# Optimization experiments

Measured on AMD Instinct MI355X. Metric: run time of the kernel, lower is better.

Reference implementation:

```python
import jax, jax.numpy as jnp
import numpy as np

DIM = 384
HEADS = 12
HEAD_DIM = DIM // HEADS
SCALE = HEAD_DIM ** -0.5
HIDDEN = 4 * DIM
EPS = 1e-5


def _dwconv(x, w, b):
    # depthwise 3x3 conv, NCHW, kernel [C,1,3,3], groups=C
    y = jax.lax.conv_general_dilated(
        x, w, window_strides=(1, 1), padding='SAME',
        dimension_numbers=('NCHW', 'OIHW', 'NCHW'),
        feature_group_count=x.shape[1])
    return y + b[None, :, None, None]


def _layernorm(x, g, b):
    mu = jnp.mean(x, axis=-1, keepdims=True)
    var = jnp.mean(jnp.square(x - mu), axis=-1, keepdims=True)
    return (x - mu) * jax.lax.rsqrt(var + EPS) * g + b


def setup_inputs() -> dict:
    key = jax.random.key(0)
    ks = jax.random.split(key, 10)
    s = 0.02
    inp = {
        'x': jax.random.normal(ks[0], (32, DIM, 28, 28), dtype=jnp.float32),
        'cpe1_w': jax.random.normal(ks[1], (DIM, 1, 3, 3), dtype=jnp.float32) * s,
        'cpe1_b': jnp.zeros((DIM,), jnp.float32),
        'norm1_g': jnp.ones((DIM,), jnp.float32),
        'norm1_b': jnp.zeros((DIM,), jnp.float32),
        'qkv_w': jax.random.normal(ks[2], (3 * DIM, DIM), dtype=jnp.float32) * s,
        'proj_w': jax.random.normal(ks[3], (DIM, DIM), dtype=jnp.float32) * s,
        'proj_b': jnp.zeros((DIM,), jnp.float32),
        'cpe2_w': jax.random.normal(ks[4], (DIM, 1, 3, 3), dtype=jnp.float32) * s,
        'cpe2_b': jnp.zeros((DIM,), jnp.float32),
        'norm2_g': jnp.ones((DIM,), jnp.float32),
        'norm2_b': jnp.zeros((DIM,), jnp.float32),
        'fc1_w': jax.random.normal(ks[5], (HIDDEN, DIM), dtype=jnp.float32) * s,
        'fc1_b': jnp.zeros((HIDDEN,), jnp.float32),
        'fc2_w': jax.random.normal(ks[6], (DIM, HIDDEN), dtype=jnp.float32) * s,
        'fc2_b': jnp.zeros((DIM,), jnp.float32),
    }
    return inp


def reference(x, cpe1_w, cpe1_b, norm1_g, norm1_b, qkv_w, proj_w, proj_b,
              cpe2_w, cpe2_b, norm2_g, norm2_b, fc1_w, fc1_b, fc2_w, fc2_b):
    B, C, H, W = x.shape
    N = H * W
    # cpe1: depthwise conv residual (act = Identity)
    x = x + _dwconv(x, cpe1_w, cpe1_b)
    x = jnp.transpose(x.reshape(B, C, N), (0, 2, 1))  # [B, N, C]

    # channel attention
    cur = _layernorm(x, norm1_g, norm1_b)
    qkv = cur @ qkv_w.T  # [B, N, 3C]
    qkv = qkv.reshape(B, N, 3, HEADS, HEAD_DIM)
    q = qkv[:, :, 0]  # [B, N, h, d]
    k = qkv[:, :, 1] * SCALE
    v = qkv[:, :, 2]
    # attn = k^T @ v over tokens: [B, h, d, d]
    attn = jnp.einsum('bnhd,bnhe->bhde', k, v)
    attn = jax.nn.softmax(attn, axis=-1)
    # out[n,d] = sum_e attn[d,e] * q[n,e]
    out = jnp.einsum('bhde,bnhe->bnhd', attn, q).reshape(B, N, C)
    cur = out @ proj_w.T + proj_b
    x = x + cur

    # cpe2
    x = jnp.transpose(x, (0, 2, 1)).reshape(B, C, H, W)
    x = x + _dwconv(x, cpe2_w, cpe2_b)

    # MLP
    x = jnp.transpose(x.reshape(B, C, N), (0, 2, 1))  # [B, N, C]
    y = _layernorm(x, norm2_g, norm2_b)
    y = jax.nn.gelu(y @ fc1_w.T + fc1_b, approximate=False)
    y = y @ fc2_w.T + fc2_b
    x = x + y
    return jnp.transpose(x, (0, 2, 1)).reshape(B, C, H, W)
```

## Files before the change

### kernel.cpp

```cpp
#include <hip/hip_runtime.h>
#include <hip/hip_bf16.h>

#define CDIM 384
#define NHEADS 12
#define HDIM 32
#define HIDDEN 1536
#define BBATCH 32
#define HH 28
#define WW 28
#define NTOK 784
#define BN (BBATCH * NTOK)
#define LN_EPS 1e-5f
#define ATT_SCALE 0.17677669529663687f
#define YTILES 196
#define PERXCD 25

typedef __hip_bfloat16 bf16;
typedef __attribute__((ext_vector_type(8))) short bf16x8;
typedef __attribute__((ext_vector_type(4))) float f32x4;

__device__ __forceinline__ void stf(float* p, float v) { *p = v; }
__device__ __forceinline__ void stf(bf16* p, float v) { *p = __float2bfloat16(v); }

__device__ __forceinline__ short f2bs(float v) {
    bf16 t = __float2bfloat16(v);
    return *reinterpret_cast<short*>(&t);
}

__device__ __forceinline__ float gelu_f(float x) {
    float u = x * (0.7978845608f + 0.0356774081f * x * x);
    float e = __expf(-2.f * u);
    return x / (1.f + e);
}

__device__ __forceinline__ void gload16(const void* g, void* l) {
    __builtin_amdgcn_global_load_lds(
        (const __attribute__((address_space(1))) unsigned int*)g,
        (__attribute__((address_space(3))) unsigned int*)l, 16, 0, 0);
}

__global__ __launch_bounds__(256) void prep_k(
    const float* __restrict__ w0, const float* __restrict__ w1,
    const float* __restrict__ w2, const float* __restrict__ w3,
    bf16* __restrict__ dst, const float* __restrict__ cw,
    float* __restrict__ cwt)
{
    int blk = blockIdx.x;
    if (blk >= 6912) {
        int i = (blk - 6912) * 256 + threadIdx.x;
        if (i < 9 * CDIM) {
            int k = i / CDIM, c = i % CDIM;
            cwt[i] = cw[c * 9 + k];
        }
        return;
    }
    int i = blk * 256 + threadIdx.x;
    const float* src; int off;
    if (i < 442368)       { src = w0; off = i; }
    else if (i < 589824)  { src = w1; off = i - 442368; }
    else if (i < 1179648) { src = w2; off = i - 589824; }
    else                  { src = w3; off = i - 1179648; }
    dst[i] = __float2bfloat16(src[off]);
}

__global__ __launch_bounds__(256) void dwconv_nchw_plane(
    const float* __restrict__ x, const float* __restrict__ w,
    const float* __restrict__ bias, float* __restrict__ y)
{
    __shared__ float sm[NTOK];
    int bc = blockIdx.x;
    int c = bc % CDIM;
    const float* xp = x + (size_t)bc * NTOK;
    int tid = threadIdx.x;
#pragma unroll
    for (int i = 0; i < 4; i++) {
        int p = tid + i * 256;
        if (p < NTOK) sm[p] = xp[p];
    }
    __syncthreads();
    const float* wp = w + c * 9;
    float w00 = wp[0], w01 = wp[1], w02 = wp[2];
    float w10 = wp[3], w11 = wp[4], w12 = wp[5];
    float w20 = wp[6], w21 = wp[7], w22 = wp[8];
    float bc_ = bias[c];
    float* yp = y + (size_t)bc * NTOK;
#pragma unroll
    for (int i = 0; i < 4; i++) {
        int p = tid + i * 256;
        if (p >= NTOK) break;
        int h = p / WW, wcol = p % WW;
        bool hm = h > 0, hp = h < HH - 1, wm = wcol > 0, wpv = wcol < WW - 1;
        float s = w11 * sm[p];
        if (hm)        s += w01 * sm[p - WW];
        if (hp)        s += w21 * sm[p + WW];
        if (wm)        s += w10 * sm[p - 1];
        if (wpv)       s += w12 * sm[p + 1];
        if (hm && wm)  s += w00 * sm[p - WW - 1];
        if (hm && wpv) s += w02 * sm[p - WW + 1];
        if (hp && wm)  s += w20 * sm[p + WW - 1];
        if (hp && wpv) s += w22 * sm[p + WW + 1];
        yp[p] = sm[p] + s + bc_;
    }
}

__global__ __launch_bounds__(256) void transpose_in(
    const float* __restrict__ in, float* __restrict__ out)
{
    __shared__ float t[32][33];
    int b = blockIdx.z;
    int n0 = blockIdx.y * 32;
    int c0 = blockIdx.x * 32;
    int tx = threadIdx.x, ty = threadIdx.y;
    for (int i = ty; i < 32; i += 8) {
        int n = n0 + tx;
        if (n < NTOK) t[i][tx] = in[((size_t)b * CDIM + c0 + i) * NTOK + n];
    }
    __syncthreads();
    for (int i = ty; i < 32; i += 8) {
        int n = n0 + i;
        if (n < NTOK) out[((size_t)b * NTOK + n) * CDIM + c0 + tx] = t[tx][i];
    }
}

template <typename TO>
__global__ __launch_bounds__(256) void layernorm_k(
    const float* __restrict__ in, const float* __restrict__ g,
    const float* __restrict__ b, TO* __restrict__ out)
{
    int wid = threadIdx.x >> 6;
    int lane = threadIdx.x & 63;
    size_t r = (size_t)blockIdx.x * 4 + wid;
    const float* row = in + r * CDIM;
    float v[6];
    float s = 0.f;
#pragma unroll
    for (int j = 0; j < 6; j++) { v[j] = row[lane + 64 * j]; s += v[j]; }
#pragma unroll
    for (int off = 32; off >= 1; off >>= 1) s += __shfl_xor(s, off);
    float mu = s * (1.f / CDIM);
    float q = 0.f;
#pragma unroll
    for (int j = 0; j < 6; j++) { float d = v[j] - mu; q += d * d; }
#pragma unroll
    for (int off = 32; off >= 1; off >>= 1) q += __shfl_xor(q, off);
    float rs = rsqrtf(q * (1.f / CDIM) + LN_EPS);
    TO* orow = out + r * CDIM;
#pragma unroll
    for (int j = 0; j < 6; j++) {
        int c = lane + 64 * j;
        stf(&orow[c], (v[j] - mu) * rs * g[c] + b[c]);
    }
}

__global__ __launch_bounds__(256) void cpe2_ln_fused(
    const float* __restrict__ xin, const float* __restrict__ wt,
    const float* __restrict__ cbias, const float* __restrict__ g,
    const float* __restrict__ b, float* __restrict__ x3,
    bf16* __restrict__ lnout)
{
    __shared__ float wts[9 * CDIM];
    int tid = threadIdx.x;
    for (int i = tid; i < 9 * CDIM; i += 256) wts[i] = wt[i];
    __syncthreads();
    int wid = tid >> 6, lane = tid & 63;
    int tok = blockIdx.x * 4 + wid;
    int n = tok % NTOK;
    int h = n / WW, w = n % WW;
    bool hm = h > 0, hp = h < HH - 1, wm = w > 0, wpv = w < WW - 1;
    const float* row = xin + (size_t)tok * CDIM;
    float ctr[6], acc6[6], val[6];
#pragma unroll
    for (int j = 0; j < 6; j++) {
        int c = lane + 64 * j;
        ctr[j] = row[c];
        acc6[j] = wts[4 * CDIM + c] * ctr[j];
    }
#define TAP(k, cond, dn)                                                      \
    if (cond) {                                                               \
        const float* rp = row + (dn) * CDIM;                                  \
        _Pragma("unroll")                                                     \
        for (int j = 0; j < 6; j++) {                                         \
            int c = lane + 64 * j;                                            \
            acc6[j] = fmaf(wts[(k) * CDIM + c], rp[c], acc6[j]);              \
        }                                                                     \
    }
    TAP(0, hm && wm,   -WW - 1)
    TAP(1, hm,         -WW)
    TAP(2, hm && wpv,  -WW + 1)
    TAP(3, wm,         -1)
    TAP(5, wpv,        1)
    TAP(6, hp && wm,   WW - 1)
    TAP(7, hp,         WW)
    TAP(8, hp && wpv,  WW + 1)
#undef TAP
    float s = 0.f;
    float* x3row = x3 + (size_t)tok * CDIM;
#pragma unroll
    for (int j = 0; j < 6; j++) {
        int c = lane + 64 * j;
        val[j] = ctr[j] + acc6[j] + cbias[c];
        x3row[c] = val[j];
        s += val[j];
    }
#pragma unroll
    for (int off = 32; off >= 1; off >>= 1) s += __shfl_xor(s, off);
    float mu = s * (1.f / CDIM);
    float q = 0.f;
#pragma unroll
    for (int j = 0; j < 6; j++) { float d = val[j] - mu; q += d * d; }
#pragma unroll
    for (int off = 32; off >= 1; off >>= 1) q += __shfl_xor(q, off);
    float rs = rsqrtf(q * (1.f / CDIM) + LN_EPS);
    bf16* orow = lnout + (size_t)tok * CDIM;
#pragma unroll
    for (int j = 0; j < 6; j++) {
        int c = lane + 64 * j;
        orow[c] = __float2bfloat16((val[j] - mu) * rs * g[c] + b[c]);
    }
}

template <int ACT, bool RES, typename TO, bool OUTT, int K>
__global__ __launch_bounds__(256, 4) void gemm_mfma(
    const short* __restrict__ Abf, const short* __restrict__ Bw,
    const float* __restrict__ bias, const float* __restrict__ res,
    TO* __restrict__ Co, int M, int NX)
{
    int id = blockIdx.x;
    int xcd = id & 7, slot_ = id >> 3;
    int yloc = slot_ / NX, xx = slot_ - yloc * NX;
    int y = xcd * PERXCD + yloc;
    if (y >= YTILES) return;

    __shared__ __align__(16) short lds[16896];
    const int tid = threadIdx.x;
    const int wid = tid >> 6, lane = tid & 63;
    const int wrow = wid >> 1, wcol = wid & 1;
    const int quad = lane >> 4, lr = lane & 15;
    const int r0 = y * 128, m0 = xx * 128;

    const int srow = lane >> 2;
    const int sg   = (lane & 3) ^ ((lane >> 3) & 3);
    const short* gA = Abf + (size_t)(r0 + wid * 32 + srow) * K + sg * 8;
    const short* gB = Bw  + (size_t)(m0 + wid * 32 + srow) * K + sg * 8;

    auto stage = [&](int k0, int p) {
        short* lA = lds + p * 8192 + wid * 1024;
        short* lB = lds + p * 8192 + 4096 + wid * 1024;
#pragma unroll
        for (int k = 0; k < 2; k++) {
            gload16(gA + k0 + (size_t)k * 16 * K, lA + k * 512);
            gload16(gB + k0 + (size_t)k * 16 * K, lB + k * 512);
        }
    };

    const int slot = (quad ^ ((lr >> 1) & 3)) * 8;
    int fA[4], fB[4];
#pragma unroll
    for (int i = 0; i < 4; i++) {
        fA[i] = (wrow * 64 + i * 16 + lr) * 32 + slot;
        fB[i] = 4096 + (wcol * 64 + i * 16 + lr) * 32 + slot;
    }

    f32x4 acc[4][4] = {};

    stage(0, 0);
    int p = 0;
    for (int k0 = 0; k0 < K; k0 += 32) {
        __syncthreads();
        if (k0 + 32 < K) stage(k0 + 32, p ^ 1);
        const short* As = lds + p * 8192;
        bf16x8 av[4], bv[4];
#pragma unroll
        for (int i = 0; i < 4; i++) {
            av[i] = *(const bf16x8*)(As + fA[i]);
            bv[i] = *(const bf16x8*)(As + fB[i]);
        }
#pragma unroll
        for (int i = 0; i < 4; i++)
#pragma unroll
            for (int j = 0; j < 4; j++)
                acc[i][j] = __builtin_amdgcn_mfma_f32_16x16x32_bf16(
                    av[i], bv[j], acc[i][j], 0, 0, 0);
        p ^= 1;
    }

    if constexpr (OUTT) {
        float* Csf = (float*)lds;
        __syncthreads();
#pragma unroll
        for (int pass = 0; pass < 2; pass++) {
            if (wcol == pass) {
#pragma unroll
                for (int i = 0; i < 4; i++) {
                    int lrow = wrow * 64 + i * 16 + quad * 4;
#pragma unroll
                    for (int j = 0; j < 4; j++) {
                        int lcol = j * 16 + lr;
                        int gc = m0 + pass * 64 + lcol;
                        float bb = bias ? bias[gc] : 0.f;
#pragma unroll
                        for (int rr = 0; rr < 4; rr++) {
                            float v = acc[i][j][rr] + bb;
                            if (RES)
                                v += res[(size_t)(r0 + lrow + rr) * M + gc];
                            if (ACT == 1) v = gelu_f(v);
                            Csf[(lrow + rr) * 66 + lcol] = v;
                        }
                    }
                }
            }
            __syncthreads();
            int tok = tid & 127;
            int csel = tid >> 7;
            int gtok = r0 + tok;
            int bb2 = gtok / NTOK;
            int nn2 = gtok - bb2 * NTOK;
#pragma unroll
            for (int s = 0; s < 32; s++) {
                int cl = s * 2 + csel;
                int gcol = m0 + pass * 64 + cl;
                Co[((size_t)bb2 * CDIM + gcol) * NTOK + nn2] = Csf[tok * 66 + cl];
            }
            __syncthreads();
        }
    } else if constexpr (sizeof(TO) == 4) {
#pragma unroll
        for (int i = 0; i < 4; i++) {
            int gr = r0 + wrow * 64 + i * 16 + quad * 4;
#pragma unroll
            for (int j = 0; j < 4; j++) {
                int gc = m0 + wcol * 64 + j * 16 + lr;
                float bb = bias ? bias[gc] : 0.f;
#pragma unroll
                for (int rr = 0; rr < 4; rr++) {
                    size_t idx = (size_t)(gr + rr) * M + gc;
                    float v = acc[i][j][rr] + bb;
                    if (RES) v += res[idx];
                    if (ACT == 1) v = gelu_f(v);
                    stf((float*)&Co[idx], v);
                }
            }
        }
    } else {
        __syncthreads();
        short* Cs = lds;
#pragma unroll
        for (int i = 0; i < 4; i++) {
            int lrow = wrow * 64 + i * 16 + quad * 4;
#pragma unroll
            for (int j = 0; j < 4; j++) {
                int lcol = wcol * 64 + j * 16 + lr;
                float bb = bias ? bias[m0 + lcol] : 0.f;
#pragma unroll
                for (int rr = 0; rr < 4; rr++) {
                    float v = acc[i][j][rr] + bb;
                    if (ACT == 1) v = gelu_f(v);
                    Cs[(lrow + rr) * 132 + lcol] = f2bs(v);
                }
            }
        }
        __syncthreads();
        short* co = (short*)Co;
#pragma unroll
        for (int s = 0; s < 16; s++) {
            int row = s * 8 + (tid >> 5);
            int seg = tid & 31;
            uint2 vv = *(const uint2*)(Cs + row * 132 + seg * 4);
            *(uint2*)(co + (size_t)(r0 + row) * M + m0 + seg * 4) = vv;
        }
    }
}

__global__ __launch_bounds__(256) void attn_k(
    const bf16* __restrict__ qkv, float* __restrict__ attn)
{
    int bh = blockIdx.x;
    int b = bh / NHEADS, h = bh % NHEADS;
    __shared__ float ks[64][32];
    __shared__ float vs[64][32];
    __shared__ float sm[32][33];
    int tid = threadIdx.x;
    int d = tid >> 3, e0 = (tid & 7) * 4;
    float acc[4] = {0.f, 0.f, 0.f, 0.f};
    for (int n0 = 0; n0 < NTOK; n0 += 64) {
#pragma unroll
        for (int i = 0; i < 8; i++) {
            int idx = tid + i * 256;
            int nn = idx >> 5, cc = idx & 31;
            int n = n0 + nn;
            float kv = 0.f, vv = 0.f;
            if (n < NTOK) {
                size_t base = ((size_t)b * NTOK + n) * (3 * CDIM);
                kv = ATT_SCALE * __bfloat162float(qkv[base + CDIM + h * HDIM + cc]);
                vv = __bfloat162float(qkv[base + 2 * CDIM + h * HDIM + cc]);
            }
            ks[nn][cc] = kv; vs[nn][cc] = vv;
        }
        __syncthreads();
#pragma unroll 8
        for (int nn = 0; nn < 64; nn++) {
            float kd = ks[nn][d];
            float4 vv4 = *(const float4*)&vs[nn][e0];
            acc[0] = fmaf(kd, vv4.x, acc[0]);
            acc[1] = fmaf(kd, vv4.y, acc[1]);
            acc[2] = fmaf(kd, vv4.z, acc[2]);
            acc[3] = fmaf(kd, vv4.w, acc[3]);
        }
        __syncthreads();
    }
#pragma unroll
    for (int j = 0; j < 4; j++) sm[d][e0 + j] = acc[j];
    __syncthreads();
    if (tid < 32) {
        float mx = -1e30f;
#pragma unroll
        for (int e = 0; e < 32; e++) mx = fmaxf(mx, sm[tid][e]);
        float ssum = 0.f;
        float ex[32];
#pragma unroll
        for (int e = 0; e < 32; e++) { ex[e] = expf(sm[tid][e] - mx); ssum += ex[e]; }
        float inv = 1.f / ssum;
        float* arow = attn + ((size_t)bh * 32 + tid) * 32;
#pragma unroll
        for (int e = 0; e < 32; e++) arow[e] = ex[e] * inv;
    }
}

__global__ __launch_bounds__(384) void apply_attn_k(
    const bf16* __restrict__ qkv, const float* __restrict__ attn,
    bf16* __restrict__ out)
{
    int b = blockIdx.x;
    int chunk = blockIdx.y;
    int tid = threadIdx.x;
    int h = tid >> 5;
    __shared__ float qs[8][CDIM];
    float at[32];
    const float4* ap = (const float4*)(attn + ((size_t)(b * NHEADS) * 32 + tid) * 32);
#pragma unroll
    for (int e4 = 0; e4 < 8; e4++) {
        float4 v = ap[e4];
        at[e4 * 4 + 0] = v.x; at[e4 * 4 + 1] = v.y;
        at[e4 * 4 + 2] = v.z; at[e4 * 4 + 3] = v.w;
    }
    int nbase = chunk * 56;
    for (int t0 = 0; t0 < 56; t0 += 8) {
        __syncthreads();
#pragma unroll
        for (int i = 0; i < 8; i++) {
            int n = nbase + t0 + i;
            qs[i][tid] = __bfloat162float(qkv[((size_t)b * NTOK + n) * (3 * CDIM) + tid]);
        }
        __syncthreads();
#pragma unroll
        for (int i = 0; i < 8; i++) {
            const float4* q4 = (const float4*)&qs[i][h * 32];
            float s = 0.f;
#pragma unroll
            for (int e4 = 0; e4 < 8; e4++) {
                float4 qv = q4[e4];
                s = fmaf(at[e4 * 4 + 0], qv.x, s);
                s = fmaf(at[e4 * 4 + 1], qv.y, s);
                s = fmaf(at[e4 * 4 + 2], qv.z, s);
                s = fmaf(at[e4 * 4 + 3], qv.w, s);
            }
            int n = nbase + t0 + i;
            out[((size_t)b * NTOK + n) * CDIM + tid] = __float2bfloat16(s);
        }
    }
}

extern "C" void kernel_launch(void* const* d_in, const int* in_sizes, int n_in,
                              void* d_out, int out_size, void* d_ws, size_t ws_size,
                              hipStream_t stream) {
    const float* x      = (const float*)d_in[0];
    const float* cpe1_w = (const float*)d_in[1];
    const float* cpe1_b = (const float*)d_in[2];
    const float* n1g    = (const float*)d_in[3];
    const float* n1b    = (const float*)d_in[4];
    const float* qkv_w  = (const float*)d_in[5];
    const float* proj_w = (const float*)d_in[6];
    const float* proj_b = (const float*)d_in[7];
    const float* cpe2_w = (const float*)d_in[8];
    const float* cpe2_b = (const float*)d_in[9];
    const float* n2g    = (const float*)d_in[10];
    const float* n2b    = (const float*)d_in[11];
    const float* fc1_w  = (const float*)d_in[12];
    const float* fc1_b  = (const float*)d_in[13];
    const float* fc2_w  = (const float*)d_in[14];
    const float* fc2_b  = (const float*)d_in[15];

    const size_t A = (size_t)BN * CDIM;
    const size_t HA = A / 2;

    bf16* wqkv  = (bf16*)d_ws;
    bf16* wproj = wqkv + 442368;
    bf16* wfc1  = wproj + 147456;
    bf16* wfc2  = wfc1 + 589824;
    float* base = (float*)d_ws + 884736;

    float* xt        = base;
    bf16*  curb      = (bf16*)(base + A);
    bf16*  ylnb      = (bf16*)(base + A);
    bf16*  qkvb      = (bf16*)(base + A + HA);
    float* x3        = base + A + HA;
    bf16*  h1        = (bf16*)(base + A + HA + A);
    float* attnm     = base + 3 * A;
    bf16*  attn_outb = (bf16*)(base + 3 * A + 393216);
    float* xconv     = base + (A * 7) / 2;
    float* cpe2_wt   = base + (A * 9) / 2;

    const int GEMM_GRID3  = 8 * PERXCD * 3;
    const int GEMM_GRID9  = 8 * PERXCD * 9;
    const int GEMM_GRID12 = 8 * PERXCD * 12;

    prep_k<<<6926, 256, 0, stream>>>(qkv_w, proj_w, fc1_w, fc2_w, wqkv,
                                     cpe2_w, cpe2_wt);

    dwconv_nchw_plane<<<BBATCH * CDIM, 256, 0, stream>>>(x, cpe1_w, cpe1_b, xconv);
    transpose_in<<<dim3(CDIM / 32, (NTOK + 31) / 32, BBATCH), dim3(32, 8), 0, stream>>>(
        xconv, xt);
    layernorm_k<bf16><<<BN / 4, 256, 0, stream>>>(xt, n1g, n1b, curb);
    gemm_mfma<0, false, bf16, false, 384><<<GEMM_GRID9, 256, 0, stream>>>(
        (const short*)curb, (const short*)wqkv, nullptr, nullptr, qkvb, 1152, 9);
    attn_k<<<BBATCH * NHEADS, 256, 0, stream>>>(qkvb, attnm);
    apply_attn_k<<<dim3(BBATCH, 14), 384, 0, stream>>>(qkvb, attnm, attn_outb);
    gemm_mfma<0, true, float, false, 384><<<GEMM_GRID3, 256, 0, stream>>>(
        (const short*)attn_outb, (const short*)wproj, proj_b, xt, xt, 384, 3);
    cpe2_ln_fused<<<BN / 4, 256, 0, stream>>>(xt, cpe2_wt, cpe2_b, n2g, n2b,
                                              x3, ylnb);
    gemm_mfma<1, false, bf16, false, 384><<<GEMM_GRID12, 256, 0, stream>>>(
        (const short*)ylnb, (const short*)wfc1, fc1_b, nullptr, h1, 1536, 12);
    gemm_mfma<0, true, float, true, 1536><<<GEMM_GRID3, 256, 0, stream>>>(
        (const short*)h1, (const short*)wfc2, fc2_b, x3, (float*)d_out, 384, 3);
}
```

Measured before the change: 438.5 us.

## Fuse cpe1 conv with transpose and vectorize LN, cpe2, attention loads

Merges the first depthwise conv into the NCHW-to-NHWC transpose kernel by loading a 96-token halo window per channel into shared memory, which removes the intermediate xconv buffer round trip and one launch. LayerNorm1 and the cpe2+LN kernel switch to half-wave rows with float4 loads and packed bf16 stores. The attention reduction and attention-apply kernels now load bf16 K/V/Q in 16-byte vectors and convert with shifts. The cost is extra halo reads and branchy conv work in the transpose kernel.

```diff
diff --git a/kernel.cpp b/kernel.cpp
--- a/kernel.cpp
+++ b/kernel.cpp
@@ -27,6 +27,10 @@
     return *reinterpret_cast<short*>(&t);
 }
 
+__device__ __forceinline__ float bf2f(unsigned short u) {
+    return __uint_as_float(((unsigned)u) << 16);
+}
+
 __device__ __forceinline__ float gelu_f(float x) {
     float u = x * (0.7978845608f + 0.0356774081f * x * x);
     float e = __expf(-2.f * u);
@@ -63,92 +67,95 @@
     dst[i] = __float2bfloat16(src[off]);
 }
 
-__global__ __launch_bounds__(256) void dwconv_nchw_plane(
+__global__ __launch_bounds__(256) void cpe1_tr_fused(
     const float* __restrict__ x, const float* __restrict__ w,
-    const float* __restrict__ bias, float* __restrict__ y)
-{
-    __shared__ float sm[NTOK];
-    int bc = blockIdx.x;
-    int c = bc % CDIM;
-    const float* xp = x + (size_t)bc * NTOK;
-    int tid = threadIdx.x;
-#pragma unroll
-    for (int i = 0; i < 4; i++) {
-        int p = tid + i * 256;
-        if (p < NTOK) sm[p] = xp[p];
-    }
-    __syncthreads();
-    const float* wp = w + c * 9;
-    float w00 = wp[0], w01 = wp[1], w02 = wp[2];
-    float w10 = wp[3], w11 = wp[4], w12 = wp[5];
-    float w20 = wp[6], w21 = wp[7], w22 = wp[8];
-    float bc_ = bias[c];
-    float* yp = y + (size_t)bc * NTOK;
-#pragma unroll
-    for (int i = 0; i < 4; i++) {
-        int p = tid + i * 256;
-        if (p >= NTOK) break;
-        int h = p / WW, wcol = p % WW;
-        bool hm = h > 0, hp = h < HH - 1, wm = wcol > 0, wpv = wcol < WW - 1;
-        float s = w11 * sm[p];
-        if (hm)        s += w01 * sm[p - WW];
-        if (hp)        s += w21 * sm[p + WW];
-        if (wm)        s += w10 * sm[p - 1];
-        if (wpv)       s += w12 * sm[p + 1];
-        if (hm && wm)  s += w00 * sm[p - WW - 1];
-        if (hm && wpv) s += w02 * sm[p - WW + 1];
-        if (hp && wm)  s += w20 * sm[p + WW - 1];
-        if (hp && wpv) s += w22 * sm[p + WW + 1];
-        yp[p] = sm[p] + s + bc_;
-    }
-}
-
-__global__ __launch_bounds__(256) void transpose_in(
-    const float* __restrict__ in, float* __restrict__ out)
-{
+    const float* __restrict__ bias, float* __restrict__ xt)
+{
+    __shared__ float sm[32][100];
     __shared__ float t[32][33];
     int b = blockIdx.z;
     int n0 = blockIdx.y * 32;
     int c0 = blockIdx.x * 32;
     int tx = threadIdx.x, ty = threadIdx.y;
-    for (int i = ty; i < 32; i += 8) {
-        int n = n0 + tx;
-        if (n < NTOK) t[i][tx] = in[((size_t)b * CDIM + c0 + i) * NTOK + n];
+    int wstart = n0 - 32;
+    for (int ci = ty; ci < 32; ci += 8) {
+        const float* bp = x + ((size_t)b * CDIM + c0 + ci) * NTOK;
+#pragma unroll
+        for (int j = 0; j < 3; j++) {
+            int l = tx + j * 32;
+            int n = wstart + l;
+            sm[ci][l] = ((unsigned)n < NTOK) ? bp[n] : 0.f;
+        }
+    }
+    __syncthreads();
+    int n = n0 + tx;
+    if (n < NTOK) {
+        int h = n / WW, wc = n % WW;
+        bool hm = h > 0, hp = h < HH - 1, wm = wc > 0, wpv = wc < WW - 1;
+        int l = tx + 32;
+        for (int ci = ty; ci < 32; ci += 8) {
+            const float* wp = w + (c0 + ci) * 9;
+            float s = wp[4] * sm[ci][l];
+            if (hm)        s += wp[1] * sm[ci][l - WW];
+            if (hp)        s += wp[7] * sm[ci][l + WW];
+            if (wm)        s += wp[3] * sm[ci][l - 1];
+            if (wpv)       s += wp[5] * sm[ci][l + 1];
+            if (hm && wm)  s += wp[0] * sm[ci][l - WW - 1];
+            if (hm && wpv) s += wp[2] * sm[ci][l - WW + 1];
+            if (hp && wm)  s += wp[6] * sm[ci][l + WW - 1];
+            if (hp && wpv) s += wp[8] * sm[ci][l + WW + 1];
+            t[tx][ci] = sm[ci][l] + s + bias[c0 + ci];
+        }
     }
     __syncthreads();
     for (int i = ty; i < 32; i += 8) {
-        int n = n0 + i;
-        if (n < NTOK) out[((size_t)b * NTOK + n) * CDIM + c0 + tx] = t[tx][i];
-    }
-}
-
-template <typename TO>
-__global__ __launch_bounds__(256) void layernorm_k(
+        int nn = n0 + i;
+        if (nn < NTOK)
+            xt[((size_t)b * NTOK + nn) * CDIM + c0 + tx] = t[i][tx];
+    }
+}
+
+__global__ __launch_bounds__(256) void ln1_k(
     const float* __restrict__ in, const float* __restrict__ g,
-    const float* __restrict__ b, TO* __restrict__ out)
-{
-    int wid = threadIdx.x >> 6;
-    int lane = threadIdx.x & 63;
-    size_t r = (size_t)blockIdx.x * 4 + wid;
-    const float* row = in + r * CDIM;
-    float v[6];
+    const float* __restrict__ b, bf16* __restrict__ out)
+{
+    int tid = threadIdx.x;
+    int l = tid & 31;
+    size_t tok = (size_t)blockIdx.x * 8 + (tid >> 5);
+    const float4* row = (const float4*)(in + tok * CDIM);
+    float4 v[3];
     float s = 0.f;
 #pragma unroll
-    for (int j = 0; j < 6; j++) { v[j] = row[lane + 64 * j]; s += v[j]; }
-#pragma unroll
-    for (int off = 32; off >= 1; off >>= 1) s += __shfl_xor(s, off);
+    for (int j = 0; j < 3; j++) {
+        v[j] = row[l + j * 32];
+        s += v[j].x + v[j].y + v[j].z + v[j].w;
+    }
+#pragma unroll
+    for (int off = 16; off >= 1; off >>= 1) s += __shfl_xor(s, off);
     float mu = s * (1.f / CDIM);
     float q = 0.f;
 #pragma unroll
-    for (int j = 0; j < 6; j++) { float d = v[j] - mu; q += d * d; }
-#pragma unroll
-    for (int off = 32; off >= 1; off >>= 1) q += __shfl_xor(q, off);
+    for (int j = 0; j < 3; j++) {
+        float dx = v[j].x - mu, dy = v[j].y - mu;
+        float dz = v[j].z - mu, dw = v[j].w - mu;
+        q += dx * dx + dy * dy + dz * dz + dw * dw;
+    }
+#pragma unroll
+    for (int off = 16; off >= 1; off >>= 1) q += __shfl_xor(q, off);
     float rs = rsqrtf(q * (1.f / CDIM) + LN_EPS);
-    TO* orow = out + r * CDIM;
-#pragma unroll
-    for (int j = 0; j < 6; j++) {
-        int c = lane + 64 * j;
-        stf(&orow[c], (v[j] - mu) * rs * g[c] + b[c]);
+    const float4* g4 = (const float4*)g;
+    const float4* b4 = (const float4*)b;
+    ushort4* o4 = (ushort4*)(out + tok * CDIM);
+#pragma unroll
+    for (int j = 0; j < 3; j++) {
+        int idx = l + j * 32;
+        float4 gv = g4[idx], bv = b4[idx];
+        ushort4 r;
+        r.x = (unsigned short)f2bs((v[j].x - mu) * rs * gv.x + bv.x);
+        r.y = (unsigned short)f2bs((v[j].y - mu) * rs * gv.y + bv.y);
+        r.z = (unsigned short)f2bs((v[j].z - mu) * rs * gv.z + bv.z);
+        r.w = (unsigned short)f2bs((v[j].w - mu) * rs * gv.w + bv.w);
+        o4[idx] = r;
     }
 }
 
@@ -160,29 +167,38 @@
 {
     __shared__ float wts[9 * CDIM];
     int tid = threadIdx.x;
-    for (int i = tid; i < 9 * CDIM; i += 256) wts[i] = wt[i];
+    for (int i = tid; i < 864; i += 256)
+        ((float4*)wts)[i] = ((const float4*)wt)[i];
     __syncthreads();
-    int wid = tid >> 6, lane = tid & 63;
-    int tok = blockIdx.x * 4 + wid;
-    int n = tok % NTOK;
-    int h = n / WW, w = n % WW;
-    bool hm = h > 0, hp = h < HH - 1, wm = w > 0, wpv = w < WW - 1;
-    const float* row = xin + (size_t)tok * CDIM;
-    float ctr[6], acc6[6], val[6];
-#pragma unroll
-    for (int j = 0; j < 6; j++) {
-        int c = lane + 64 * j;
-        ctr[j] = row[c];
-        acc6[j] = wts[4 * CDIM + c] * ctr[j];
-    }
-#define TAP(k, cond, dn)                                                      \
-    if (cond) {                                                               \
-        const float* rp = row + (dn) * CDIM;                                  \
-        _Pragma("unroll")                                                     \
-        for (int j = 0; j < 6; j++) {                                         \
-            int c = lane + 64 * j;                                            \
-            acc6[j] = fmaf(wts[(k) * CDIM + c], rp[c], acc6[j]);              \
-        }                                                                     \
+    int l = tid & 31;
+    size_t tok = (size_t)blockIdx.x * 8 + (tid >> 5);
+    int n = (int)(tok % NTOK);
+    int h = n / WW, wc = n % WW;
+    bool hm = h > 0, hp = h < HH - 1, wm = wc > 0, wpv = wc < WW - 1;
+    const float* row = xin + tok * CDIM;
+    const float4* w4 = (const float4*)wts;
+    float4 ctr[3], acc[3];
+#pragma unroll
+    for (int j = 0; j < 3; j++) {
+        int idx = l + j * 32;
+        ctr[j] = ((const float4*)row)[idx];
+        float4 ww = w4[4 * 96 + idx];
+        acc[j].x = ww.x * ctr[j].x; acc[j].y = ww.y * ctr[j].y;
+        acc[j].z = ww.z * ctr[j].z; acc[j].w = ww.w * ctr[j].w;
+    }
+#define TAP(k, cond, dn)                                                     \
+    if (cond) {                                                              \
+        const float4* rp = (const float4*)(row + (dn) * CDIM);               \
+        _Pragma("unroll")                                                    \
+        for (int j = 0; j < 3; j++) {                                        \
+            int idx = l + j * 32;                                            \
+            float4 vv = rp[idx];                                             \
+            float4 ww = w4[(k) * 96 + idx];                                  \
+            acc[j].x = fmaf(ww.x, vv.x, acc[j].x);                           \
+            acc[j].y = fmaf(ww.y, vv.y, acc[j].y);                           \
+            acc[j].z = fmaf(ww.z, vv.z, acc[j].z);                           \
+            acc[j].w = fmaf(ww.w, vv.w, acc[j].w);                           \
+        }                                                                    \
     }
     TAP(0, hm && wm,   -WW - 1)
     TAP(1, hm,         -WW)
@@ -194,28 +210,45 @@
     TAP(8, hp && wpv,  WW + 1)
 #undef TAP
     float s = 0.f;
-    float* x3row = x3 + (size_t)tok * CDIM;
-#pragma unroll
-    for (int j = 0; j < 6; j++) {
-        int c = lane + 64 * j;
-        val[j] = ctr[j] + acc6[j] + cbias[c];
-        x3row[c] = val[j];
-        s += val[j];
-    }
-#pragma unroll
-    for (int off = 32; off >= 1; off >>= 1) s += __shfl_xor(s, off);
+    float4 val[3];
+    float4* x3r = (float4*)(x3 + tok * CDIM);
+#pragma unroll
+    for (int j = 0; j < 3; j++) {
+        int idx = l + j * 32;
+        float4 cb = ((const float4*)cbias)[idx];
+        val[j].x = ctr[j].x + acc[j].x + cb.x;
+        val[j].y = ctr[j].y + acc[j].y + cb.y;
+        val[j].z = ctr[j].z + acc[j].z + cb.z;
+        val[j].w = ctr[j].w + acc[j].w + cb.w;
+        x3r[idx] = val[j];
+        s += val[j].x + val[j].y + val[j].z + val[j].w;
+    }
+#pragma unroll
+    for (int off = 16; off >= 1; off >>= 1) s += __shfl_xor(s, off);
     float mu = s * (1.f / CDIM);
     float q = 0.f;
 #pragma unroll
-    for (int j = 0; j < 6; j++) { float d = val[j] - mu; q += d * d; }
-#pragma unroll
-    for (int off = 32; off >= 1; off >>= 1) q += __shfl_xor(q, off);
+    for (int j = 0; j < 3; j++) {
+        float dx = val[j].x - mu, dy = val[j].y - mu;
+        float dz = val[j].z - mu, dw = val[j].w - mu;
+        q += dx * dx + dy * dy + dz * dz + dw * dw;
+    }
+#pragma unroll
+    for (int off = 16; off >= 1; off >>= 1) q += __shfl_xor(q, off);
     float rs = rsqrtf(q * (1.f / CDIM) + LN_EPS);
-    bf16* orow = lnout + (size_t)tok * CDIM;
-#pragma unroll
-    for (int j = 0; j < 6; j++) {
-        int c = lane + 64 * j;
-        orow[c] = __float2bfloat16((val[j] - mu) * rs * g[c] + b[c]);
+    const float4* g4 = (const float4*)g;
+    const float4* b4 = (const float4*)b;
+    ushort4* o4 = (ushort4*)(lnout + tok * CDIM);
+#pragma unroll
+    for (int j = 0; j < 3; j++) {
+        int idx = l + j * 32;
+        float4 gv = g4[idx], bv = b4[idx];
+        ushort4 r;
+        r.x = (unsigned short)f2bs((val[j].x - mu) * rs * gv.x + bv.x);
+        r.y = (unsigned short)f2bs((val[j].y - mu) * rs * gv.y + bv.y);
+        r.z = (unsigned short)f2bs((val[j].z - mu) * rs * gv.z + bv.z);
+        r.w = (unsigned short)f2bs((val[j].w - mu) * rs * gv.w + bv.w);
+        o4[idx] = r;
     }
 }
 
@@ -381,26 +414,36 @@
     __shared__ float sm[32][33];
     int tid = threadIdx.x;
     int d = tid >> 3, e0 = (tid & 7) * 4;
+    int nn = tid >> 2, q8 = (tid & 3) * 8;
     float acc[4] = {0.f, 0.f, 0.f, 0.f};
     for (int n0 = 0; n0 < NTOK; n0 += 64) {
-#pragma unroll
-        for (int i = 0; i < 8; i++) {
-            int idx = tid + i * 256;
-            int nn = idx >> 5, cc = idx & 31;
-            int n = n0 + nn;
-            float kv = 0.f, vv = 0.f;
-            if (n < NTOK) {
-                size_t base = ((size_t)b * NTOK + n) * (3 * CDIM);
-                kv = ATT_SCALE * __bfloat162float(qkv[base + CDIM + h * HDIM + cc]);
-                vv = __bfloat162float(qkv[base + 2 * CDIM + h * HDIM + cc]);
+        int n = n0 + nn;
+        float kv[8], vv[8];
+        if (n < NTOK) {
+            const unsigned short* base =
+                (const unsigned short*)qkv + ((size_t)b * NTOK + n) * (3 * CDIM);
+            uint4 kq = *(const uint4*)(base + CDIM + h * HDIM + q8);
+            uint4 vq = *(const uint4*)(base + 2 * CDIM + h * HDIM + q8);
+            const unsigned short* kp = (const unsigned short*)&kq;
+            const unsigned short* vp = (const unsigned short*)&vq;
+#pragma unroll
+            for (int j = 0; j < 8; j++) {
+                kv[j] = ATT_SCALE * bf2f(kp[j]);
+                vv[j] = bf2f(vp[j]);
             }
-            ks[nn][cc] = kv; vs[nn][cc] = vv;
-        }
+        } else {
+#pragma unroll
+            for (int j = 0; j < 8; j++) { kv[j] = 0.f; vv[j] = 0.f; }
+        }
+        *(float4*)&ks[nn][q8]     = make_float4(kv[0], kv[1], kv[2], kv[3]);
+        *(float4*)&ks[nn][q8 + 4] = make_float4(kv[4], kv[5], kv[6], kv[7]);
+        *(float4*)&vs[nn][q8]     = make_float4(vv[0], vv[1], vv[2], vv[3]);
+        *(float4*)&vs[nn][q8 + 4] = make_float4(vv[4], vv[5], vv[6], vv[7]);
         __syncthreads();
 #pragma unroll 8
-        for (int nn = 0; nn < 64; nn++) {
-            float kd = ks[nn][d];
-            float4 vv4 = *(const float4*)&vs[nn][e0];
+        for (int k = 0; k < 64; k++) {
+            float kd = ks[k][d];
+            float4 vv4 = *(const float4*)&vs[k][e0];
             acc[0] = fmaf(kd, vv4.x, acc[0]);
             acc[1] = fmaf(kd, vv4.y, acc[1]);
             acc[2] = fmaf(kd, vv4.z, acc[2]);
@@ -443,13 +486,21 @@
         at[e4 * 4 + 0] = v.x; at[e4 * 4 + 1] = v.y;
         at[e4 * 4 + 2] = v.z; at[e4 * 4 + 3] = v.w;
     }
+    int row8 = tid / 48;
+    int seg = tid - row8 * 48;
     int nbase = chunk * 56;
     for (int t0 = 0; t0 < 56; t0 += 8) {
         __syncthreads();
-#pragma unroll
-        for (int i = 0; i < 8; i++) {
-            int n = nbase + t0 + i;
-            qs[i][tid] = __bfloat162float(qkv[((size_t)b * NTOK + n) * (3 * CDIM) + tid]);
+        {
+            int n = nbase + t0 + row8;
+            const unsigned short* src =
+                (const unsigned short*)qkv + ((size_t)b * NTOK + n) * (3 * CDIM) + seg * 8;
+            uint4 qv = *(const uint4*)src;
+            const unsigned short* qp = (const unsigned short*)&qv;
+            *(float4*)&qs[row8][seg * 8] =
+                make_float4(bf2f(qp[0]), bf2f(qp[1]), bf2f(qp[2]), bf2f(qp[3]));
+            *(float4*)&qs[row8][seg * 8 + 4] =
+                make_float4(bf2f(qp[4]), bf2f(qp[5]), bf2f(qp[6]), bf2f(qp[7]));
         }
         __syncthreads();
 #pragma unroll
@@ -507,7 +558,6 @@
     bf16*  h1        = (bf16*)(base + A + HA + A);
     float* attnm     = base + 3 * A;
     bf16*  attn_outb = (bf16*)(base + 3 * A + 393216);
-    float* xconv     = base + (A * 7) / 2;
     float* cpe2_wt   = base + (A * 9) / 2;
 
     const int GEMM_GRID3  = 8 * PERXCD * 3;
@@ -517,17 +567,16 @@
     prep_k<<<6926, 256, 0, stream>>>(qkv_w, proj_w, fc1_w, fc2_w, wqkv,
                                      cpe2_w, cpe2_wt);
 
-    dwconv_nchw_plane<<<BBATCH * CDIM, 256, 0, stream>>>(x, cpe1_w, cpe1_b, xconv);
-    transpose_in<<<dim3(CDIM / 32, (NTOK + 31) / 32, BBATCH), dim3(32, 8), 0, stream>>>(
-        xconv, xt);
-    layernorm_k<bf16><<<BN / 4, 256, 0, stream>>>(xt, n1g, n1b, curb);
+    cpe1_tr_fused<<<dim3(CDIM / 32, 25, BBATCH), dim3(32, 8), 0, stream>>>(
+        x, cpe1_w, cpe1_b, xt);
+    ln1_k<<<BN / 8, 256, 0, stream>>>(xt, n1g, n1b, curb);
     gemm_mfma<0, false, bf16, false, 384><<<GEMM_GRID9, 256, 0, stream>>>(
         (const short*)curb, (const short*)wqkv, nullptr, nullptr, qkvb, 1152, 9);
     attn_k<<<BBATCH * NHEADS, 256, 0, stream>>>(qkvb, attnm);
     apply_attn_k<<<dim3(BBATCH, 14), 384, 0, stream>>>(qkvb, attnm, attn_outb);
     gemm_mfma<0, true, float, false, 384><<<GEMM_GRID3, 256, 0, stream>>>(
         (const short*)attn_outb, (const short*)wproj, proj_b, xt, xt, 384, 3);
-    cpe2_ln_fused<<<BN / 4, 256, 0, stream>>>(xt, cpe2_wt, cpe2_b, n2g, n2b,
+    cpe2_ln_fused<<<BN / 8, 256, 0, stream>>>(xt, cpe2_wt, cpe2_b, n2g, n2b,
                                               x3, ylnb);
     gemm_mfma<1, false, bf16, false, 384><<<GEMM_GRID12, 256, 0, stream>>>(
         (const short*)ylnb, (const short*)wfc1, fc1_b, nullptr, h1, 1536, 12);
```

Measured after the change: 434.2 us. No clear change (-1.0%).
